# Kernel optimization log

Measured on AMD Instinct MI355X. Metric: run time of the kernel, lower is better.

The kernel has to match this reference:

```python
import jax, jax.numpy as jnp
import numpy as np

N = 4096
IN_DIM = 256
OUT_DIM = 256
NUM_HEADS = 4
HEAD_DIM = OUT_DIM // NUM_HEADS


def setup_inputs() -> dict:
    key = jax.random.key(0)
    ks = jax.random.split(key, 10)
    x = jax.random.normal(ks[0], (N, IN_DIM), dtype=jnp.float32)
    adj = jax.random.randint(ks[1], (N, N), 0, 2, dtype=jnp.int32)
    adj = jnp.maximum(adj, jnp.eye(N, dtype=jnp.int32))  # self-loops -> no empty rows
    s_in = 1.0 / np.sqrt(IN_DIM)
    s_out = 1.0 / np.sqrt(OUT_DIM)
    Wq = jax.random.uniform(ks[2], (IN_DIM, OUT_DIM), jnp.float32, -s_in, s_in)
    bq = jnp.zeros((OUT_DIM,), jnp.float32)
    Wk = jax.random.uniform(ks[3], (IN_DIM, OUT_DIM), jnp.float32, -s_in, s_in)
    bk = jnp.zeros((OUT_DIM,), jnp.float32)
    Wv = jax.random.uniform(ks[4], (IN_DIM, OUT_DIM), jnp.float32, -s_in, s_in)
    bv = jnp.zeros((OUT_DIM,), jnp.float32)
    Wo = jax.random.uniform(ks[5], (OUT_DIM, OUT_DIM), jnp.float32, -s_out, s_out)
    bo = jnp.zeros((OUT_DIM,), jnp.float32)
    gamma = jnp.ones((OUT_DIM,), jnp.float32)
    beta = jnp.zeros((OUT_DIM,), jnp.float32)
    return {"x": x, "adj": adj, "Wq": Wq, "bq": bq, "Wk": Wk, "bk": bk,
            "Wv": Wv, "bv": bv, "Wo": Wo, "bo": bo, "gamma": gamma, "beta": beta}


def layer_norm(h, gamma, beta, eps=1e-5):
    mu = jnp.mean(h, axis=-1, keepdims=True)
    var = jnp.mean(jnp.square(h - mu), axis=-1, keepdims=True)
    return (h - mu) * jax.lax.rsqrt(var + eps) * gamma + beta


def reference(x, adj, Wq, bq, Wk, bk, Wv, bv, Wo, bo, gamma, beta):
    n = x.shape[0]
    q_proj = x @ Wq + bq                       # (N, out_dim), reused for residual
    Q = q_proj.reshape(n, NUM_HEADS, HEAD_DIM)
    K = (x @ Wk + bk).reshape(n, NUM_HEADS, HEAD_DIM)
    V = (x @ Wv + bv).reshape(n, NUM_HEADS, HEAD_DIM)
    scores = jnp.einsum('nhd,mhd->nmh', Q, K) / np.sqrt(HEAD_DIM)
    scores = jnp.where(adj[:, :, None] == 0, -jnp.inf, scores)
    attn = jax.nn.softmax(scores, axis=1)      # softmax over neighbor axis m
    out = jnp.einsum('nmh,mhd->nhd', attn, V).reshape(n, OUT_DIM)
    out = out @ Wo + bo
    return layer_norm(out + q_proj, gamma, beta)
```

## Files before the change

### kernel.cpp

```cpp
#include <hip/hip_runtime.h>
#include <math.h>

#define NN 4096
#define DIM 256
#define NHEADS 4
#define HDIM 64

typedef short bf16x8 __attribute__((ext_vector_type(8)));
typedef float f32x4  __attribute__((ext_vector_type(4)));

__device__ __forceinline__ unsigned short f2bf(float f) {
    unsigned int u = __float_as_uint(f);
    u += 0x7fffu + ((u >> 16) & 1u);
    return (unsigned short)(u >> 16);
}
__device__ __forceinline__ float bf2f(unsigned short h) {
    return __uint_as_float(((unsigned int)h) << 16);
}
__device__ __forceinline__ void async16(const void* g, void* l) {
    __builtin_amdgcn_global_load_lds(
        (const __attribute__((address_space(1))) unsigned int*)g,
        (__attribute__((address_space(3))) unsigned int*)l, 16, 0, 0);
}

__global__ __launch_bounds__(256)
void prep_kernel(const float* __restrict__ W0, const float* __restrict__ W1,
                 const float* __restrict__ W2, const float* __restrict__ W3,
                 unsigned short* __restrict__ T0, unsigned short* __restrict__ T1,
                 unsigned short* __restrict__ T2, unsigned short* __restrict__ T3)
{
    __shared__ unsigned short Ts[64][65];
    const int b = blockIdx.x, t = threadIdx.x;
    const int mat = b >> 4, tile = b & 15;
    const int r0 = (tile >> 2) * 64, c0 = (tile & 3) * 64;
    const float* W = (mat == 0) ? W0 : (mat == 1) ? W1 : (mat == 2) ? W2 : W3;
    unsigned short* T = (mat == 0) ? T0 : (mat == 1) ? T1 : (mat == 2) ? T2 : T3;
    {
        int r = t >> 2, c4 = (t & 3) * 16;
        #pragma unroll
        for (int j = 0; j < 4; ++j) {
            float4 v = *reinterpret_cast<const float4*>(W + (size_t)(r0 + r) * DIM + c0 + c4 + j * 4);
            Ts[c4 + j * 4 + 0][r] = f2bf(v.x);
            Ts[c4 + j * 4 + 1][r] = f2bf(v.y);
            Ts[c4 + j * 4 + 2][r] = f2bf(v.z);
            Ts[c4 + j * 4 + 3][r] = f2bf(v.w);
        }
    }
    __syncthreads();
    {
        int d = t >> 2, k4 = (t & 3) * 16;
        #pragma unroll
        for (int j = 0; j < 4; ++j) {
            ushort4 u;
            u.x = Ts[d][k4 + j * 4 + 0];
            u.y = Ts[d][k4 + j * 4 + 1];
            u.z = Ts[d][k4 + j * 4 + 2];
            u.w = Ts[d][k4 + j * 4 + 3];
            *reinterpret_cast<ushort4*>(T + (size_t)(c0 + d) * DIM + r0 + k4 + j * 4) = u;
        }
    }
}

__global__ __launch_bounds__(256)
void qkv_mask(const float* __restrict__ x,
              const unsigned short* __restrict__ WqT, const unsigned short* __restrict__ WkT,
              const unsigned short* __restrict__ WvT,
              const float* __restrict__ bq, const float* __restrict__ bk, const float* __restrict__ bv,
              unsigned short* __restrict__ Qo, unsigned short* __restrict__ Ko,
              unsigned short* __restrict__ VTo,
              const int* __restrict__ adj, unsigned long long* __restrict__ maskT)
{
    const int b = blockIdx.x, t = threadIdx.x, w = t >> 6, l = t & 63;

    if (b >= 384) {
        const int ww = (b - 384) * 4 + w;
        for (int idx = ww; idx < 65536; idx += 8192) {
            const int row = idx >> 4, st = idx & 15;
            const int* ap = adj + (size_t)row * NN + st * 256 + l;
            const int a0 = ap[0];
            const int a1 = ap[64];
            const int a2 = ap[128];
            const int a3 = ap[192];
            unsigned long long b0 = __ballot(a0 != 0);
            unsigned long long b1 = __ballot(a1 != 0);
            unsigned long long b2 = __ballot(a2 != 0);
            unsigned long long b3 = __ballot(a3 != 0);
            if (l < 4) {
                unsigned long long bb = (l == 0) ? b0 : (l == 1) ? b1 : (l == 2) ? b2 : b3;
                maskT[(size_t)row * 64 + st * 4 + l] = bb;
            }
        }
        return;
    }

    const int l15 = l & 15, lg = l >> 4;
    const int which = b >> 7, xb = b & 127;
    const int row0 = xb * 32 + (w >> 1) * 16;
    const int col0 = (w & 1) * 128;
    const unsigned short* WT; const float* bias;
    if (which == 0)      { WT = WqT; bias = bq; }
    else if (which == 1) { WT = WkT; bias = bk; }
    else                 { WT = WvT; bias = bv; }

    f32x4 acc[8] = {};
    for (int k0 = 0; k0 < DIM; k0 += 32) {
        const float* xp = x + (size_t)(row0 + l15) * DIM + k0 + lg * 8;
        float4 x0 = *reinterpret_cast<const float4*>(xp);
        float4 x1 = *reinterpret_cast<const float4*>(xp + 4);
        union { unsigned u[4]; bf16x8 v; } xa;
        asm("v_cvt_pk_bf16_f32 %0, %1, %2" : "=v"(xa.u[0]) : "v"(x0.x), "v"(x0.y));
        asm("v_cvt_pk_bf16_f32 %0, %1, %2" : "=v"(xa.u[1]) : "v"(x0.z), "v"(x0.w));
        asm("v_cvt_pk_bf16_f32 %0, %1, %2" : "=v"(xa.u[2]) : "v"(x1.x), "v"(x1.y));
        asm("v_cvt_pk_bf16_f32 %0, %1, %2" : "=v"(xa.u[3]) : "v"(x1.z), "v"(x1.w));
        #pragma unroll
        for (int nt = 0; nt < 8; ++nt) {
            bf16x8 wb = *(const bf16x8*)(WT + (size_t)(col0 + nt * 16 + l15) * DIM + k0 + lg * 8);
            acc[nt] = __builtin_amdgcn_mfma_f32_16x16x32_bf16(xa.v, wb, acc[nt], 0, 0, 0);
        }
    }
    #pragma unroll
    for (int nt = 0; nt < 8; ++nt) {
        int col = col0 + nt * 16 + l15;
        float bb = bias[col];
        #pragma unroll
        for (int r = 0; r < 4; ++r) {
            int row = row0 + lg * 4 + r;
            float ov = acc[nt][r] + bb;
            if (which == 1) ov *= 0.18033688f;
            unsigned short val = f2bf(ov);
            if (which == 2) {
                int rb = row & 63;
                int vnt = rb >> 4, vlg = (rb >> 2) & 3, vr = rb & 3;
                int pos = ((vnt & 1) << 5) | (vlg << 3) | ((vnt >> 1) << 2) | vr;
                VTo[(size_t)col * NN + ((row & ~63) | pos)] = val;
            } else if (which == 0) Qo[(size_t)row * DIM + col] = val;
            else                   Ko[(size_t)row * DIM + col] = val;
        }
    }
}

template<int NTILES>
__global__ __launch_bounds__(512, 4)
void attn_mfma(const unsigned short* __restrict__ Qb, const unsigned short* __restrict__ Kb,
               const unsigned short* __restrict__ VT, const unsigned long long* __restrict__ maskT,
               unsigned short* __restrict__ Opart, float* __restrict__ lpart)
{
    constexpr int NSTR = NTILES / 4;
    __shared__ unsigned short Kt[2][64][64];
    __shared__ unsigned short Vt[2][64][64];

    const int t = threadIdx.x, w = t >> 6, l = t & 63, l15 = l & 15, lg = l >> 4;
    const int bid = blockIdx.x;
    const int slice = (bid & 7) + 8 * (bid >> 8);
    const int qb    = (bid >> 3) & 31;
    const int h  = slice & 3;
    const int sp = slice >> 2;
    const int kv_base = sp * NTILES * 64;
    const int qrow = qb * 128 + w * 16;

    const unsigned short* qp = Qb + (size_t)(qrow + l15) * DIM + h * HDIM + lg * 8;
    const bf16x8 qa0 = *(const bf16x8*)(qp);
    const bf16x8 qa1 = *(const bf16x8*)(qp + 32);

    const unsigned long long* mbase = maskT + (size_t)(qrow + l15) * 64 + (kv_base >> 6);

    const int srow  = w * 8 + (l >> 3);
    const int sunit = (l & 7) ^ (srow & 7);
    const unsigned short* kS = Kb + (size_t)(kv_base + srow) * DIM + h * HDIM + sunit * 8;
    const unsigned short* vS = VT + (size_t)(h * HDIM + srow) * NN + kv_base + sunit * 8;

    const int xr  = l15 & 7;
    const int ko0 = (lg ^ xr) << 4;
    const int ko1 = ((4 + lg) ^ xr) << 4;

    const short onev = (l15 == 0) ? (short)0x3F80 : (short)0;
    const bf16x8 onesb = {onev, onev, onev, onev, onev, onev, onev, onev};

    f32x4 oa[4] = {};
    f32x4 os = {};

    {
        async16(kS, &Kt[0][w * 8][0]);
        async16(vS, &Vt[0][w * 8][0]);
    }

    #pragma unroll 1
    for (int st = 0; st < NSTR; ++st) {
        const ulonglong4 m4 = *reinterpret_cast<const ulonglong4*>(mbase + st * 4);

        #pragma unroll
        for (int m = 0; m < 4; ++m) {
            const int tl = st * 4 + m;
            asm volatile("s_waitcnt vmcnt(0)" ::: "memory");
            __builtin_amdgcn_s_barrier();
            __builtin_amdgcn_sched_barrier(0);

            if (tl + 1 < NTILES) {
                const int bb = (tl + 1) & 1;
                async16(kS + (size_t)(tl + 1) * 64 * DIM, &Kt[bb][w * 8][0]);
                async16(vS + (tl + 1) * 64,               &Vt[bb][w * 8][0]);
            }

            const int cb = tl & 1;
            const char* kbase = (const char*)&Kt[cb][0][0] + l15 * 128;
            const char* vbase = (const char*)&Vt[cb][0][0] + l15 * 128;

            f32x4 sa[4] = {};
            __builtin_amdgcn_s_setprio(1);
            #pragma unroll
            for (int nt = 0; nt < 4; ++nt) {
                bf16x8 kb0 = *(const bf16x8*)(kbase + nt * 2048 + ko0);
                bf16x8 kb1 = *(const bf16x8*)(kbase + nt * 2048 + ko1);
                sa[nt] = __builtin_amdgcn_mfma_f32_16x16x32_bf16(kb0, qa0, sa[nt], 0, 0, 0);
                sa[nt] = __builtin_amdgcn_mfma_f32_16x16x32_bf16(kb1, qa1, sa[nt], 0, 0, 0);
            }
            __builtin_amdgcn_s_setprio(0);

            const unsigned long long w64 =
                (m == 0) ? m4.x : (m == 1) ? m4.y : (m == 2) ? m4.z : m4.w;
            const unsigned long long sh = w64 >> (lg * 4);
            const unsigned shlo = (unsigned)sh, shhi = (unsigned)(sh >> 32);
            float p[4][4];
            #pragma unroll
            for (int nt = 0; nt < 4; ++nt) {
                #pragma unroll
                for (int r = 0; r < 4; ++r) {
                    const int bitpos = nt * 16 + r;
                    const unsigned word = (bitpos < 32) ? shlo : shhi;
                    const unsigned bit = (word >> (bitpos & 31)) & 1u;
                    p[nt][r] = exp2f(bit ? sa[nt][r] : -INFINITY);
                }
            }
            union { unsigned u[4]; bf16x8 v; } a0, a1;
            asm("v_cvt_pk_bf16_f32 %0, %1, %2" : "=v"(a0.u[0]) : "v"(p[0][0]), "v"(p[0][1]));
            asm("v_cvt_pk_bf16_f32 %0, %1, %2" : "=v"(a0.u[1]) : "v"(p[0][2]), "v"(p[0][3]));
            asm("v_cvt_pk_bf16_f32 %0, %1, %2" : "=v"(a0.u[2]) : "v"(p[2][0]), "v"(p[2][1]));
            asm("v_cvt_pk_bf16_f32 %0, %1, %2" : "=v"(a0.u[3]) : "v"(p[2][2]), "v"(p[2][3]));
            asm("v_cvt_pk_bf16_f32 %0, %1, %2" : "=v"(a1.u[0]) : "v"(p[1][0]), "v"(p[1][1]));
            asm("v_cvt_pk_bf16_f32 %0, %1, %2" : "=v"(a1.u[1]) : "v"(p[1][2]), "v"(p[1][3]));
            asm("v_cvt_pk_bf16_f32 %0, %1, %2" : "=v"(a1.u[2]) : "v"(p[3][0]), "v"(p[3][1]));
            asm("v_cvt_pk_bf16_f32 %0, %1, %2" : "=v"(a1.u[3]) : "v"(p[3][2]), "v"(p[3][3]));
            const bf16x8 pa0 = a0.v;
            const bf16x8 pa1 = a1.v;

            __builtin_amdgcn_s_setprio(1);
            #pragma unroll
            for (int nt = 0; nt < 4; ++nt) {
                bf16x8 vb0 = *(const bf16x8*)(vbase + nt * 2048 + ko0);
                bf16x8 vb1 = *(const bf16x8*)(vbase + nt * 2048 + ko1);
                oa[nt] = __builtin_amdgcn_mfma_f32_16x16x32_bf16(pa0, vb0, oa[nt], 0, 0, 0);
                oa[nt] = __builtin_amdgcn_mfma_f32_16x16x32_bf16(pa1, vb1, oa[nt], 0, 0, 0);
            }
            os = __builtin_amdgcn_mfma_f32_16x16x32_bf16(pa0, onesb, os, 0, 0, 0);
            os = __builtin_amdgcn_mfma_f32_16x16x32_bf16(pa1, onesb, os, 0, 0, 0);
            __builtin_amdgcn_s_setprio(0);
        }
    }

    #pragma unroll
    for (int r = 0; r < 4; ++r) {
        const int qr = qrow + lg * 4 + r;
        #pragma unroll
        for (int nt = 0; nt < 4; ++nt)
            Opart[((size_t)sp * NN + qr) * DIM + h * HDIM + nt * 16 + l15] = f2bf(oa[nt][r]);
        if (l15 == 0)
            lpart[((size_t)sp * NN + qr) * NHEADS + h] = os[r];
    }
}

__global__ __launch_bounds__(256)
void out_ln_fused(const unsigned short* __restrict__ Opart, const float* __restrict__ lpart,
                  const unsigned short* __restrict__ WoT, const float* __restrict__ bo,
                  const unsigned short* __restrict__ Rb, const float* __restrict__ gamma,
                  const float* __restrict__ beta, float* __restrict__ out, int S)
{
    __shared__ unsigned short As[16][264];
    __shared__ float redsum[4][16];
    __shared__ float redsq[4][16];
    const int t = threadIdx.x, w = t >> 6, l = t & 63, l15 = l & 15, lg = l >> 4;
    const int row0 = blockIdx.x * 16;

    {
        const int row = t >> 4;
        const int d0  = (t & 15) * 16;
        const int hh  = d0 >> 6;
        float lsum = 0.f;
        for (int s = 0; s < S; ++s)
            lsum += lpart[((size_t)s * NN + row0 + row) * NHEADS + hh];
        const float inv = 1.f / lsum;
        float a16[16] = {};
        for (int s = 0; s < S; ++s) {
            const unsigned short* op = Opart + ((size_t)s * NN + row0 + row) * DIM + d0;
            #pragma unroll
            for (int j4 = 0; j4 < 4; ++j4) {
                ushort4 u = *reinterpret_cast<const ushort4*>(op + j4 * 4);
                a16[j4 * 4 + 0] += bf2f(u.x);
                a16[j4 * 4 + 1] += bf2f(u.y);
                a16[j4 * 4 + 2] += bf2f(u.z);
                a16[j4 * 4 + 3] += bf2f(u.w);
            }
        }
        #pragma unroll
        for (int j4 = 0; j4 < 4; ++j4) {
            ushort4 ov;
            ov.x = f2bf(a16[j4 * 4 + 0] * inv);
            ov.y = f2bf(a16[j4 * 4 + 1] * inv);
            ov.z = f2bf(a16[j4 * 4 + 2] * inv);
            ov.w = f2bf(a16[j4 * 4 + 3] * inv);
            *reinterpret_cast<ushort4*>(&As[row][d0 + j4 * 4]) = ov;
        }
    }
    __syncthreads();

    const int col0 = w * 64;
    f32x4 acc[4] = {};
    for (int k0 = 0; k0 < DIM; k0 += 32) {
        bf16x8 xa = *reinterpret_cast<const bf16x8*>(&As[l15][k0 + lg * 8]);
        #pragma unroll
        for (int nt = 0; nt < 4; ++nt) {
            bf16x8 wb = *(const bf16x8*)(WoT + (size_t)(col0 + nt * 16 + l15) * DIM + k0 + lg * 8);
            acc[nt] = __builtin_amdgcn_mfma_f32_16x16x32_bf16(xa, wb, acc[nt], 0, 0, 0);
        }
    }

    float psum[4] = {0, 0, 0, 0}, psq[4] = {0, 0, 0, 0};
    #pragma unroll
    for (int nt = 0; nt < 4; ++nt) {
        int col = col0 + nt * 16 + l15;
        float bb = bo[col];
        #pragma unroll
        for (int r = 0; r < 4; ++r) {
            int row = row0 + lg * 4 + r;
            float xv = acc[nt][r] + bb + bf2f(Rb[(size_t)row * DIM + col]);
            acc[nt][r] = xv;
            psum[r] += xv; psq[r] += xv * xv;
        }
    }
    #pragma unroll
    for (int r = 0; r < 4; ++r) {
        float s = psum[r], q = psq[r];
        s += __shfl_xor(s, 1); q += __shfl_xor(q, 1);
        s += __shfl_xor(s, 2); q += __shfl_xor(q, 2);
        s += __shfl_xor(s, 4); q += __shfl_xor(q, 4);
        s += __shfl_xor(s, 8); q += __shfl_xor(q, 8);
        psum[r] = s; psq[r] = q;
    }
    if (l15 == 0) {
        #pragma unroll
        for (int r = 0; r < 4; ++r) {
            redsum[w][lg * 4 + r] = psum[r];
            redsq[w][lg * 4 + r]  = psq[r];
        }
    }
    __syncthreads();

    float msave[4], rsave[4];
    #pragma unroll
    for (int r = 0; r < 4; ++r) {
        int row = lg * 4 + r;
        float s = redsum[0][row] + redsum[1][row] + redsum[2][row] + redsum[3][row];
        float q = redsq[0][row] + redsq[1][row] + redsq[2][row] + redsq[3][row];
        float mean = s * (1.f / 256.f);
        float var  = q * (1.f / 256.f) - mean * mean;
        msave[r] = mean;
        rsave[r] = rsqrtf(var + 1e-5f);
    }
    #pragma unroll
    for (int nt = 0; nt < 4; ++nt) {
        int col = col0 + nt * 16 + l15;
        float g = gamma[col], bt = beta[col];
        #pragma unroll
        for (int r = 0; r < 4; ++r) {
            int row = row0 + lg * 4 + r;
            out[(size_t)row * DIM + col] = (acc[nt][r] - msave[r]) * rsave[r] * g + bt;
        }
    }
}

extern "C" void kernel_launch(void* const* d_in, const int* in_sizes, int n_in,
                              void* d_out, int out_size, void* d_ws, size_t ws_size,
                              hipStream_t stream) {
    const float* x     = (const float*)d_in[0];
    const int*   adj   = (const int*)  d_in[1];
    const float* Wq    = (const float*)d_in[2];
    const float* bq    = (const float*)d_in[3];
    const float* Wk    = (const float*)d_in[4];
    const float* bk    = (const float*)d_in[5];
    const float* Wv    = (const float*)d_in[6];
    const float* bv    = (const float*)d_in[7];
    const float* Wo    = (const float*)d_in[8];
    const float* bo    = (const float*)d_in[9];
    const float* gamma = (const float*)d_in[10];
    const float* beta  = (const float*)d_in[11];
    float* out = (float*)d_out;

    char* ws = (char*)d_ws;
    const size_t MB = 1u << 20;
    unsigned short*     Qb    = (unsigned short*)(ws + 0 * MB);
    unsigned short*     Kb    = (unsigned short*)(ws + 2 * MB);
    unsigned short*     VT    = (unsigned short*)(ws + 4 * MB);
    unsigned long long* maskT = (unsigned long long*)(ws + 6 * MB);
    unsigned short*     WqT   = (unsigned short*)(ws + 8 * MB);
    unsigned short*     WkT   = (unsigned short*)(ws + 8 * MB + 128 * 1024);
    unsigned short*     WvT   = (unsigned short*)(ws + 8 * MB + 256 * 1024);
    unsigned short*     WoT   = (unsigned short*)(ws + 8 * MB + 384 * 1024);
    float*              lpart = (float*)(ws + 10 * MB + 512 * 1024);
    unsigned short*     Opart = (unsigned short*)(ws + 11 * MB);

    const int S = (ws_size >= 27 * MB) ? 8 : 4;

    prep_kernel<<<64, 256, 0, stream>>>(Wq, Wk, Wv, Wo, WqT, WkT, WvT, WoT);

    qkv_mask<<<384 + 2048, 256, 0, stream>>>(
        x, WqT, WkT, WvT, bq, bk, bv, Qb, Kb, VT, adj, maskT);

    if (S == 8)
        attn_mfma<8><<<1024, 512, 0, stream>>>(Qb, Kb, VT, maskT, Opart, lpart);
    else
        attn_mfma<16><<<512, 512, 0, stream>>>(Qb, Kb, VT, maskT, Opart, lpart);

    out_ln_fused<<<NN / 16, 256, 0, stream>>>(
        Opart, lpart, WoT, bo, Qb, gamma, beta, out, S);
}
```

Before: 84.26 us.

## Process two 16-row query subtiles per wave to reuse K/V LDS fragments

Each wave now handles 32 query rows as two 16-row subtiles, so every K and V fragment read from LDS feeds twice as many MFMAs. The query block grows from 128 to 256 rows and the grid is halved, which halves the total K/V global-to-LDS traffic and the barrier count per unit of work. The cost is doubled accumulator and score registers, which may hurt occupancy under the 512x4 launch bounds. With half as many blocks, the grid may also fill the GPU's compute units less well.

```diff
diff --git a/kernel.cpp b/kernel.cpp
--- a/kernel.cpp
+++ b/kernel.cpp
@@ -151,18 +151,23 @@
 
     const int t = threadIdx.x, w = t >> 6, l = t & 63, l15 = l & 15, lg = l >> 4;
     const int bid = blockIdx.x;
-    const int slice = (bid & 7) + 8 * (bid >> 8);
-    const int qb    = (bid >> 3) & 31;
+    const int slice = (bid & 7) + 8 * (bid >> 7);
+    const int qb    = (bid >> 3) & 15;
     const int h  = slice & 3;
     const int sp = slice >> 2;
     const int kv_base = sp * NTILES * 64;
-    const int qrow = qb * 128 + w * 16;
-
-    const unsigned short* qp = Qb + (size_t)(qrow + l15) * DIM + h * HDIM + lg * 8;
-    const bf16x8 qa0 = *(const bf16x8*)(qp);
-    const bf16x8 qa1 = *(const bf16x8*)(qp + 32);
-
-    const unsigned long long* mbase = maskT + (size_t)(qrow + l15) * 64 + (kv_base >> 6);
+    const int qrow = qb * 256 + w * 32;
+
+    bf16x8 qa[2][2];
+    #pragma unroll
+    for (int sub = 0; sub < 2; ++sub) {
+        const unsigned short* qp = Qb + (size_t)(qrow + sub * 16 + l15) * DIM + h * HDIM + lg * 8;
+        qa[sub][0] = *(const bf16x8*)(qp);
+        qa[sub][1] = *(const bf16x8*)(qp + 32);
+    }
+
+    const unsigned long long* mbase0 = maskT + (size_t)(qrow + l15) * 64 + (kv_base >> 6);
+    const unsigned long long* mbase1 = maskT + (size_t)(qrow + 16 + l15) * 64 + (kv_base >> 6);
 
     const int srow  = w * 8 + (l >> 3);
     const int sunit = (l & 7) ^ (srow & 7);
@@ -176,8 +181,8 @@
     const short onev = (l15 == 0) ? (short)0x3F80 : (short)0;
     const bf16x8 onesb = {onev, onev, onev, onev, onev, onev, onev, onev};
 
-    f32x4 oa[4] = {};
-    f32x4 os = {};
+    f32x4 oa[2][4] = {};
+    f32x4 os[2] = {};
 
     {
         async16(kS, &Kt[0][w * 8][0]);
@@ -186,7 +191,8 @@
 
     #pragma unroll 1
     for (int st = 0; st < NSTR; ++st) {
-        const ulonglong4 m4 = *reinterpret_cast<const ulonglong4*>(mbase + st * 4);
+        const ulonglong4 m40 = *reinterpret_cast<const ulonglong4*>(mbase0 + st * 4);
+        const ulonglong4 m41 = *reinterpret_cast<const ulonglong4*>(mbase1 + st * 4);
 
         #pragma unroll
         for (int m = 0; m < 4; ++m) {
@@ -205,66 +211,76 @@
             const char* kbase = (const char*)&Kt[cb][0][0] + l15 * 128;
             const char* vbase = (const char*)&Vt[cb][0][0] + l15 * 128;
 
-            f32x4 sa[4] = {};
+            f32x4 sa[2][4] = {};
             __builtin_amdgcn_s_setprio(1);
             #pragma unroll
             for (int nt = 0; nt < 4; ++nt) {
                 bf16x8 kb0 = *(const bf16x8*)(kbase + nt * 2048 + ko0);
                 bf16x8 kb1 = *(const bf16x8*)(kbase + nt * 2048 + ko1);
-                sa[nt] = __builtin_amdgcn_mfma_f32_16x16x32_bf16(kb0, qa0, sa[nt], 0, 0, 0);
-                sa[nt] = __builtin_amdgcn_mfma_f32_16x16x32_bf16(kb1, qa1, sa[nt], 0, 0, 0);
+                sa[0][nt] = __builtin_amdgcn_mfma_f32_16x16x32_bf16(kb0, qa[0][0], sa[0][nt], 0, 0, 0);
+                sa[0][nt] = __builtin_amdgcn_mfma_f32_16x16x32_bf16(kb1, qa[0][1], sa[0][nt], 0, 0, 0);
+                sa[1][nt] = __builtin_amdgcn_mfma_f32_16x16x32_bf16(kb0, qa[1][0], sa[1][nt], 0, 0, 0);
+                sa[1][nt] = __builtin_amdgcn_mfma_f32_16x16x32_bf16(kb1, qa[1][1], sa[1][nt], 0, 0, 0);
             }
             __builtin_amdgcn_s_setprio(0);
 
-            const unsigned long long w64 =
-                (m == 0) ? m4.x : (m == 1) ? m4.y : (m == 2) ? m4.z : m4.w;
-            const unsigned long long sh = w64 >> (lg * 4);
-            const unsigned shlo = (unsigned)sh, shhi = (unsigned)(sh >> 32);
-            float p[4][4];
             #pragma unroll
-            for (int nt = 0; nt < 4; ++nt) {
+            for (int sub = 0; sub < 2; ++sub) {
+                const ulonglong4& m4 = sub ? m41 : m40;
+                const unsigned long long w64 =
+                    (m == 0) ? m4.x : (m == 1) ? m4.y : (m == 2) ? m4.z : m4.w;
+                const unsigned long long shq = w64 >> (lg * 4);
+                const unsigned shlo = (unsigned)shq, shhi = (unsigned)(shq >> 32);
+                float p[4][4];
                 #pragma unroll
-                for (int r = 0; r < 4; ++r) {
-                    const int bitpos = nt * 16 + r;
-                    const unsigned word = (bitpos < 32) ? shlo : shhi;
-                    const unsigned bit = (word >> (bitpos & 31)) & 1u;
-                    p[nt][r] = exp2f(bit ? sa[nt][r] : -INFINITY);
+                for (int nt = 0; nt < 4; ++nt) {
+                    #pragma unroll
+                    for (int r = 0; r < 4; ++r) {
+                        const int bitpos = nt * 16 + r;
+                        const unsigned word = (bitpos < 32) ? shlo : shhi;
+                        const unsigned bit = (word >> (bitpos & 31)) & 1u;
+                        p[nt][r] = exp2f(bit ? sa[sub][nt][r] : -INFINITY);
+                    }
                 }
+                union { unsigned u[4]; bf16x8 v; } a0, a1;
+                asm("v_cvt_pk_bf16_f32 %0, %1, %2" : "=v"(a0.u[0]) : "v"(p[0][0]), "v"(p[0][1]));
+                asm("v_cvt_pk_bf16_f32 %0, %1, %2" : "=v"(a0.u[1]) : "v"(p[0][2]), "v"(p[0][3]));
+                asm("v_cvt_pk_bf16_f32 %0, %1, %2" : "=v"(a0.u[2]) : "v"(p[2][0]), "v"(p[2][1]));
+                asm("v_cvt_pk_bf16_f32 %0, %1, %2" : "=v"(a0.u[3]) : "v"(p[2][2]), "v"(p[2][3]));
+                asm("v_cvt_pk_bf16_f32 %0, %1, %2" : "=v"(a1.u[0]) : "v"(p[1][0]), "v"(p[1][1]));
+                asm("v_cvt_pk_bf16_f32 %0, %1, %2" : "=v"(a1.u[1]) : "v"(p[1][2]), "v"(p[1][3]));
+                asm("v_cvt_pk_bf16_f32 %0, %1, %2" : "=v"(a1.u[2]) : "v"(p[3][0]), "v"(p[3][1]));
+                asm("v_cvt_pk_bf16_f32 %0, %1, %2" : "=v"(a1.u[3]) : "v"(p[3][2]), "v"(p[3][3]));
+                const bf16x8 pa0 = a0.v;
+                const bf16x8 pa1 = a1.v;
+
+                __builtin_amdgcn_s_setprio(1);
+                #pragma unroll
+                for (int nt = 0; nt < 4; ++nt) {
+                    bf16x8 vb0 = *(const bf16x8*)(vbase + nt * 2048 + ko0);
+                    bf16x8 vb1 = *(const bf16x8*)(vbase + nt * 2048 + ko1);
+                    oa[sub][nt] = __builtin_amdgcn_mfma_f32_16x16x32_bf16(pa0, vb0, oa[sub][nt], 0, 0, 0);
+                    oa[sub][nt] = __builtin_amdgcn_mfma_f32_16x16x32_bf16(pa1, vb1, oa[sub][nt], 0, 0, 0);
+                }
+                os[sub] = __builtin_amdgcn_mfma_f32_16x16x32_bf16(pa0, onesb, os[sub], 0, 0, 0);
+                os[sub] = __builtin_amdgcn_mfma_f32_16x16x32_bf16(pa1, onesb, os[sub], 0, 0, 0);
+                __builtin_amdgcn_s_setprio(0);
             }
-            union { unsigned u[4]; bf16x8 v; } a0, a1;
-            asm("v_cvt_pk_bf16_f32 %0, %1, %2" : "=v"(a0.u[0]) : "v"(p[0][0]), "v"(p[0][1]));
-            asm("v_cvt_pk_bf16_f32 %0, %1, %2" : "=v"(a0.u[1]) : "v"(p[0][2]), "v"(p[0][3]));
-            asm("v_cvt_pk_bf16_f32 %0, %1, %2" : "=v"(a0.u[2]) : "v"(p[2][0]), "v"(p[2][1]));
-            asm("v_cvt_pk_bf16_f32 %0, %1, %2" : "=v"(a0.u[3]) : "v"(p[2][2]), "v"(p[2][3]));
-            asm("v_cvt_pk_bf16_f32 %0, %1, %2" : "=v"(a1.u[0]) : "v"(p[1][0]), "v"(p[1][1]));
-            asm("v_cvt_pk_bf16_f32 %0, %1, %2" : "=v"(a1.u[1]) : "v"(p[1][2]), "v"(p[1][3]));
-            asm("v_cvt_pk_bf16_f32 %0, %1, %2" : "=v"(a1.u[2]) : "v"(p[3][0]), "v"(p[3][1]));
-            asm("v_cvt_pk_bf16_f32 %0, %1, %2" : "=v"(a1.u[3]) : "v"(p[3][2]), "v"(p[3][3]));
-            const bf16x8 pa0 = a0.v;
-            const bf16x8 pa1 = a1.v;
-
-            __builtin_amdgcn_s_setprio(1);
+            __builtin_amdgcn_sched_barrier(0);
+        }
+    }
+
+    #pragma unroll
+    for (int sub = 0; sub < 2; ++sub) {
+        #pragma unroll
+        for (int r = 0; r < 4; ++r) {
+            const int qr = qrow + sub * 16 + lg * 4 + r;
             #pragma unroll
-            for (int nt = 0; nt < 4; ++nt) {
-                bf16x8 vb0 = *(const bf16x8*)(vbase + nt * 2048 + ko0);
-                bf16x8 vb1 = *(const bf16x8*)(vbase + nt * 2048 + ko1);
-                oa[nt] = __builtin_amdgcn_mfma_f32_16x16x32_bf16(pa0, vb0, oa[nt], 0, 0, 0);
-                oa[nt] = __builtin_amdgcn_mfma_f32_16x16x32_bf16(pa1, vb1, oa[nt], 0, 0, 0);
-            }
-            os = __builtin_amdgcn_mfma_f32_16x16x32_bf16(pa0, onesb, os, 0, 0, 0);
-            os = __builtin_amdgcn_mfma_f32_16x16x32_bf16(pa1, onesb, os, 0, 0, 0);
-            __builtin_amdgcn_s_setprio(0);
-        }
-    }
-
-    #pragma unroll
-    for (int r = 0; r < 4; ++r) {
-        const int qr = qrow + lg * 4 + r;
-        #pragma unroll
-        for (int nt = 0; nt < 4; ++nt)
-            Opart[((size_t)sp * NN + qr) * DIM + h * HDIM + nt * 16 + l15] = f2bf(oa[nt][r]);
-        if (l15 == 0)
-            lpart[((size_t)sp * NN + qr) * NHEADS + h] = os[r];
+            for (int nt = 0; nt < 4; ++nt)
+                Opart[((size_t)sp * NN + qr) * DIM + h * HDIM + nt * 16 + l15] = f2bf(oa[sub][nt][r]);
+            if (l15 == 0)
+                lpart[((size_t)sp * NN + qr) * NHEADS + h] = os[sub][r];
+        }
     }
 }
 
@@ -415,9 +431,9 @@
         x, WqT, WkT, WvT, bq, bk, bv, Qb, Kb, VT, adj, maskT);
 
     if (S == 8)
-        attn_mfma<8><<<1024, 512, 0, stream>>>(Qb, Kb, VT, maskT, Opart, lpart);
+        attn_mfma<8><<<512, 512, 0, stream>>>(Qb, Kb, VT, maskT, Opart, lpart);
     else
-        attn_mfma<16><<<512, 512, 0, stream>>>(Qb, Kb, VT, maskT, Opart, lpart);
+        attn_mfma<16><<<256, 512, 0, stream>>>(Qb, Kb, VT, maskT, Opart, lpart);
 
     out_ln_fused<<<NN / 16, 256, 0, stream>>>(
         Opart, lpart, WoT, bo, Qb, gamma, beta, out, S);
```

Result: slower. 87.84 us (+4.2%).
